# Performance work log

Measured on AMD Instinct MI355X. Metric: run time of the kernel, lower is better.

## Reference

```python
import jax, jax.numpy as jnp
import numpy as np


def setup_inputs() -> dict:
    key = jax.random.key(0)
    k1, k2, k3, k4, k5 = jax.random.split(key, 5)
    B, N, T, O, G = 32, 256, 1024, 1024, 8
    x = jax.random.normal(k1, (B, N, T), dtype=jnp.float32)
    y = jax.random.uniform(k2, (B, G), dtype=jnp.float32)  # genre mixture weights
    weight = jax.random.normal(k3, (G, O, T), dtype=jnp.float32) * (1.0 / np.sqrt(T))
    mask = jax.random.uniform(k4, (O, T), dtype=jnp.float32)
    bias = jax.random.normal(k5, (O,), dtype=jnp.float32)
    return {"x": x, "y": y, "weight": weight, "mask": mask, "bias": bias}


def reference(x, y, weight, mask, bias):
    # mask the shared weight bank: [G,O,T] * [1,O,T]
    masked_w = weight * mask[None, :, :]
    # per-sample genre-mixed weights: [B,G] x [G,O,T] -> [B,O,T]
    w_bot = jnp.einsum('bg,got->bot', y, masked_w)
    # batched masked linear: [B,N,T] x [B,O,T] -> [B,N,O], plus bias
    return jnp.einsum('bnt,bot->bno', x, w_bot) + bias
```

## Files before the change

### kernel.cpp

```cpp
#include <hip/hip_runtime.h>
#include <hip/hip_bf16.h>
#include <stdint.h>


#define B_ 32
#define N_ 256
#define T_ 1024
#define O_ 1024
#define G_ 8

#define BM 128
#define BN 128
#define BK 64

typedef __attribute__((__ext_vector_type__(8))) __bf16 bf16x8;
typedef __attribute__((__ext_vector_type__(4))) float  f32x4;

__device__ __forceinline__ unsigned short f2bf(float f) {
    union { float f; uint32_t u; } v; v.f = f;
    uint32_t u = v.u;
    uint32_t r = (u + 0x7fffu + ((u >> 16) & 1u)) >> 16;
    return (unsigned short)r;
}

#define MIX_BLOCKS (O_ * T_ / 4 / 256)
#define CVT_BLOCKS (B_ * N_ * T_ / 4 / 256)

__global__ __launch_bounds__(256) void prep_kernel(
    const float* __restrict__ w,
    const float* __restrict__ mask,
    const float* __restrict__ y,
    const float* __restrict__ x,
    unsigned short* __restrict__ Wb,
    unsigned short* __restrict__ xb)
{
    if (blockIdx.x < MIX_BLOCKS) {
        __shared__ float ys[B_ * G_];
        ys[threadIdx.x] = y[threadIdx.x];
        __syncthreads();

        const int idx = blockIdx.x * 256 + threadIdx.x;
        const int o   = idx >> 8;
        const int t4  = (idx & 255) << 2;

        const float4 m4 = *(const float4*)(mask + (size_t)o * T_ + t4);
        float4 wv[G_];
#pragma unroll
        for (int g = 0; g < G_; ++g) {
            float4 t = *(const float4*)(w + ((size_t)g * O_ + o) * T_ + t4);
            t.x *= m4.x; t.y *= m4.y; t.z *= m4.z; t.w *= m4.w;
            wv[g] = t;
        }
        unsigned short* dst = Wb + (size_t)o * T_ + t4;
#pragma unroll 4
        for (int b = 0; b < B_; ++b) {
            float ax = 0.f, ay = 0.f, az = 0.f, aw = 0.f;
#pragma unroll
            for (int g = 0; g < G_; ++g) {
                const float yv = ys[b * G_ + g];
                ax += yv * wv[g].x; ay += yv * wv[g].y;
                az += yv * wv[g].z; aw += yv * wv[g].w;
            }
            ushort4 pk;
            pk.x = f2bf(ax); pk.y = f2bf(ay); pk.z = f2bf(az); pk.w = f2bf(aw);
            *(ushort4*)(dst + (size_t)b * O_ * T_) = pk;
        }
    } else {
        const int i = (blockIdx.x - MIX_BLOCKS) * 256 + threadIdx.x;
        const float4 v = ((const float4*)x)[i];
        ushort4 pk;
        pk.x = f2bf(v.x); pk.y = f2bf(v.y); pk.z = f2bf(v.z); pk.w = f2bf(v.w);
        ((ushort4*)xb)[i] = pk;
    }
}

__device__ __forceinline__ void load16_to_lds(const unsigned short* g, unsigned short* l) {
    __builtin_amdgcn_global_load_lds(
        (const __attribute__((address_space(1))) unsigned char*)g,
        (__attribute__((address_space(3))) unsigned char*)l,
        16, 0, 0);
}

__global__ __launch_bounds__(256, 2) void gemm_kernel(
    const unsigned short* __restrict__ xb,
    const unsigned short* __restrict__ Wb,
    const float* __restrict__ bias,
    float* __restrict__ out)
{
    __shared__ __align__(16) unsigned short lA[BM * BK];
    __shared__ __align__(16) unsigned short lB[BN * BK];

    const int tn = blockIdx.x;
    const int tm = blockIdx.y;
    const int b  = blockIdx.z;

    const int tid  = threadIdx.x;
    const int lane = tid & 63;
    const int wave = tid >> 6;
    const int wm   = (wave >> 1) * 64;
    const int wn   = (wave & 1) * 64;

    const unsigned short* Ab = xb + (size_t)b * N_ * T_ + (size_t)(tm * BM) * T_;
    const unsigned short* Bb = Wb + (size_t)b * O_ * T_ + (size_t)(tn * BN) * T_;

    const int srow   = tid >> 3;
    const int schunk = (tid & 7) ^ (srow & 7);
    const unsigned short* ga0 = Ab + (size_t)srow * T_ + schunk * 8;
    const unsigned short* gb0 = Bb + (size_t)srow * T_ + schunk * 8;
    unsigned short* la_dst = lA + tid * 8;
    unsigned short* lb_dst = lB + tid * 8;

    f32x4 acc[4][4] = {};

    const int fr = lane & 15;
    const int q  = lane >> 4;
    const int sw = fr & 7;

    for (int kt = 0; kt < T_; kt += BK) {
#pragma unroll
        for (int i = 0; i < 4; ++i) {
            load16_to_lds(ga0 + kt + (size_t)(i * 32) * T_, la_dst + i * 2048);
            load16_to_lds(gb0 + kt + (size_t)(i * 32) * T_, lb_dst + i * 2048);
        }
        __syncthreads();

#pragma unroll
        for (int kk = 0; kk < 2; ++kk) {
            const int cp = ((kk * 4 + q) ^ sw) * 8;
            bf16x8 afr[4], bfr[4];
#pragma unroll
            for (int i = 0; i < 4; ++i)
                afr[i] = *(const bf16x8*)(lA + (wm + i * 16 + fr) * BK + cp);
#pragma unroll
            for (int i = 0; i < 4; ++i)
                bfr[i] = *(const bf16x8*)(lB + (wn + i * 16 + fr) * BK + cp);
#pragma unroll
            for (int mi = 0; mi < 4; ++mi)
#pragma unroll
                for (int ni = 0; ni < 4; ++ni)
                    acc[mi][ni] = __builtin_amdgcn_mfma_f32_16x16x32_bf16(
                        afr[mi], bfr[ni], acc[mi][ni], 0, 0, 0);
        }
        __syncthreads();
    }

    float* outb = out + (size_t)b * N_ * O_ + (size_t)(tm * BM) * O_ + (tn * BN);
    const int cn = lane & 15;
    const int cr = (lane >> 4) * 4;
#pragma unroll
    for (int ni = 0; ni < 4; ++ni) {
        const int col = wn + ni * 16 + cn;
        const float bv = bias[tn * BN + col];
#pragma unroll
        for (int mi = 0; mi < 4; ++mi) {
#pragma unroll
            for (int r = 0; r < 4; ++r) {
                const int row = wm + mi * 16 + cr + r;
                outb[(size_t)row * O_ + col] = acc[mi][ni][r] + bv;
            }
        }
    }
}

__global__ __launch_bounds__(256) void naive_kernel(
    const float* __restrict__ x, const float* __restrict__ y,
    const float* __restrict__ w, const float* __restrict__ mask,
    const float* __restrict__ bias, float* __restrict__ out)
{
    const int oc = blockIdx.x & 3;
    const int n  = (blockIdx.x >> 2) & (N_ - 1);
    const int b  = blockIdx.x >> 10;

    __shared__ float xs[T_];
    __shared__ float ys[G_];
    const float* xrow = x + ((size_t)b * N_ + n) * T_;
    for (int i = threadIdx.x; i < T_ / 4; i += 256)
        ((float4*)xs)[i] = ((const float4*)xrow)[i];
    if (threadIdx.x < G_) ys[threadIdx.x] = y[b * G_ + threadIdx.x];
    __syncthreads();

    const int o = oc * 256 + threadIdx.x;
    float acc = 0.f;
    for (int t = 0; t < T_; t += 4) {
        const float4 m4 = *(const float4*)(mask + (size_t)o * T_ + t);
        float4 s = {0.f, 0.f, 0.f, 0.f};
#pragma unroll
        for (int g = 0; g < G_; ++g) {
            const float4 w4 = *(const float4*)(w + ((size_t)g * O_ + o) * T_ + t);
            const float yv = ys[g];
            s.x += yv * w4.x; s.y += yv * w4.y; s.z += yv * w4.z; s.w += yv * w4.w;
        }
        acc += xs[t] * m4.x * s.x + xs[t + 1] * m4.y * s.y
             + xs[t + 2] * m4.z * s.z + xs[t + 3] * m4.w * s.w;
    }
    out[((size_t)b * N_ + n) * O_ + o] = acc + bias[o];
}

extern "C" void kernel_launch(void* const* d_in, const int* in_sizes, int n_in,
                              void* d_out, int out_size, void* d_ws, size_t ws_size,
                              hipStream_t stream) {
    const float* x    = (const float*)d_in[0];
    const float* y    = (const float*)d_in[1];
    const float* w    = (const float*)d_in[2];
    const float* mask = (const float*)d_in[3];
    const float* bias = (const float*)d_in[4];
    float* out = (float*)d_out;

    const size_t wb_bytes = (size_t)B_ * O_ * T_ * sizeof(unsigned short);
    const size_t xb_bytes = (size_t)B_ * N_ * T_ * sizeof(unsigned short);

    if (ws_size >= wb_bytes + xb_bytes) {
        unsigned short* Wb = (unsigned short*)d_ws;
        unsigned short* xb = (unsigned short*)((char*)d_ws + wb_bytes);
        prep_kernel<<<MIX_BLOCKS + CVT_BLOCKS, 256, 0, stream>>>(w, mask, y, x, Wb, xb);
        dim3 grid(O_ / BN, N_ / BM, B_);
        gemm_kernel<<<grid, 256, 0, stream>>>(xb, Wb, bias, out);
    } else {
        naive_kernel<<<B_ * N_ * (O_ / 256), 256, 0, stream>>>(x, y, w, mask, bias, out);
    }
}
```

Measured before the change: 165.3 us.

## Double-buffer GEMM LDS tiles and widen prep kernel to 8-element stores

The GEMM main loop now keeps two LDS buffers per operand and issues the global-to-LDS loads for the next K tile before computing the current one, so memory latency overlaps MFMA work. The prep kernel is reorganised so each thread handles 8 consecutive elements and writes 16-byte packed bf16 stores, and the x-conversion blocks each process 4 chunks. This launches fewer blocks. Double buffering doubles LDS use to 64KB per block, which may limit occupancy at 2 blocks per CU. The async LDS loads rely on the barrier placement for correctness.

```diff
diff --git a/kernel.cpp b/kernel.cpp
--- a/kernel.cpp
+++ b/kernel.cpp
@@ -12,6 +12,7 @@
 #define BM 128
 #define BN 128
 #define BK 64
+#define BUFSZ (BM * BK)
 
 typedef __attribute__((__ext_vector_type__(8))) __bf16 bf16x8;
 typedef __attribute__((__ext_vector_type__(4))) float  f32x4;
@@ -23,8 +24,17 @@
     return (unsigned short)r;
 }
 
-#define MIX_BLOCKS (O_ * T_ / 4 / 256)
-#define CVT_BLOCKS (B_ * N_ * T_ / 4 / 256)
+__device__ __forceinline__ uint4 pack8(const float* a) {
+    uint4 r;
+    r.x = (uint32_t)f2bf(a[0]) | ((uint32_t)f2bf(a[1]) << 16);
+    r.y = (uint32_t)f2bf(a[2]) | ((uint32_t)f2bf(a[3]) << 16);
+    r.z = (uint32_t)f2bf(a[4]) | ((uint32_t)f2bf(a[5]) << 16);
+    r.w = (uint32_t)f2bf(a[6]) | ((uint32_t)f2bf(a[7]) << 16);
+    return r;
+}
+
+#define MIXB 512
+#define CVTB 1024
 
 __global__ __launch_bounds__(256) void prep_kernel(
     const float* __restrict__ w,
@@ -34,43 +44,51 @@
     unsigned short* __restrict__ Wb,
     unsigned short* __restrict__ xb)
 {
-    if (blockIdx.x < MIX_BLOCKS) {
-        __shared__ float ys[B_ * G_];
-        ys[threadIdx.x] = y[threadIdx.x];
-        __syncthreads();
-
-        const int idx = blockIdx.x * 256 + threadIdx.x;
-        const int o   = idx >> 8;
-        const int t4  = (idx & 255) << 2;
-
-        const float4 m4 = *(const float4*)(mask + (size_t)o * T_ + t4);
-        float4 wv[G_];
+    const int tid = threadIdx.x;
+    if (blockIdx.x < MIXB) {
+        const int o = blockIdx.x * 2 + (tid >> 7);
+        const int t = (tid & 127) * 8;
+
+        const float* mp = mask + (size_t)o * T_ + t;
+        const float4 m0 = *(const float4*)(mp);
+        const float4 m1 = *(const float4*)(mp + 4);
+
+        float wv[G_][8];
 #pragma unroll
         for (int g = 0; g < G_; ++g) {
-            float4 t = *(const float4*)(w + ((size_t)g * O_ + o) * T_ + t4);
-            t.x *= m4.x; t.y *= m4.y; t.z *= m4.z; t.w *= m4.w;
-            wv[g] = t;
-        }
-        unsigned short* dst = Wb + (size_t)o * T_ + t4;
-#pragma unroll 4
+            const float* wp = w + ((size_t)g * O_ + o) * T_ + t;
+            const float4 a = *(const float4*)(wp);
+            const float4 c = *(const float4*)(wp + 4);
+            wv[g][0] = a.x * m0.x; wv[g][1] = a.y * m0.y;
+            wv[g][2] = a.z * m0.z; wv[g][3] = a.w * m0.w;
+            wv[g][4] = c.x * m1.x; wv[g][5] = c.y * m1.y;
+            wv[g][6] = c.z * m1.z; wv[g][7] = c.w * m1.w;
+        }
+        unsigned short* dst = Wb + (size_t)o * T_ + t;
         for (int b = 0; b < B_; ++b) {
-            float ax = 0.f, ay = 0.f, az = 0.f, aw = 0.f;
-#pragma unroll
-            for (int g = 0; g < G_; ++g) {
-                const float yv = ys[b * G_ + g];
-                ax += yv * wv[g].x; ay += yv * wv[g].y;
-                az += yv * wv[g].z; aw += yv * wv[g].w;
-            }
-            ushort4 pk;
-            pk.x = f2bf(ax); pk.y = f2bf(ay); pk.z = f2bf(az); pk.w = f2bf(aw);
-            *(ushort4*)(dst + (size_t)b * O_ * T_) = pk;
+            const float4 y0 = *(const float4*)(y + b * G_);
+            const float4 y1 = *(const float4*)(y + b * G_ + 4);
+            const float yv[G_] = {y0.x, y0.y, y0.z, y0.w, y1.x, y1.y, y1.z, y1.w};
+            float acc[8] = {};
+#pragma unroll
+            for (int g = 0; g < G_; ++g)
+#pragma unroll
+                for (int j = 0; j < 8; ++j)
+                    acc[j] += yv[g] * wv[g][j];
+            *(uint4*)(dst + (size_t)b * O_ * T_) = pack8(acc);
         }
     } else {
-        const int i = (blockIdx.x - MIX_BLOCKS) * 256 + threadIdx.x;
-        const float4 v = ((const float4*)x)[i];
-        ushort4 pk;
-        pk.x = f2bf(v.x); pk.y = f2bf(v.y); pk.z = f2bf(v.z); pk.w = f2bf(v.w);
-        ((ushort4*)xb)[i] = pk;
+        const int i = (blockIdx.x - MIXB) * 256 + tid;
+        const float4* x4 = (const float4*)x;
+        uint4* o4 = (uint4*)xb;
+#pragma unroll
+        for (int j = 0; j < 4; ++j) {
+            const size_t f4 = (size_t)j * 524288 + (size_t)i * 2;
+            const float4 a = x4[f4];
+            const float4 b = x4[f4 + 1];
+            const float v[8] = {a.x, a.y, a.z, a.w, b.x, b.y, b.z, b.w};
+            o4[(size_t)j * 262144 + i] = pack8(v);
+        }
     }
 }
 
@@ -87,8 +105,8 @@
     const float* __restrict__ bias,
     float* __restrict__ out)
 {
-    __shared__ __align__(16) unsigned short lA[BM * BK];
-    __shared__ __align__(16) unsigned short lB[BN * BK];
+    __shared__ __align__(16) unsigned short lA[2 * BUFSZ];
+    __shared__ __align__(16) unsigned short lB[2 * BUFSZ];
 
     const int tn = blockIdx.x;
     const int tm = blockIdx.y;
@@ -107,8 +125,17 @@
     const int schunk = (tid & 7) ^ (srow & 7);
     const unsigned short* ga0 = Ab + (size_t)srow * T_ + schunk * 8;
     const unsigned short* gb0 = Bb + (size_t)srow * T_ + schunk * 8;
-    unsigned short* la_dst = lA + tid * 8;
-    unsigned short* lb_dst = lB + tid * 8;
+
+#define STAGE(buf, kt)                                                          \
+    {                                                                           \
+        unsigned short* lad = lA + (buf) * BUFSZ + tid * 8;                     \
+        unsigned short* lbd = lB + (buf) * BUFSZ + tid * 8;                     \
+        _Pragma("unroll")                                                       \
+        for (int i_ = 0; i_ < 4; ++i_) {                                        \
+            load16_to_lds(ga0 + (kt) + (size_t)(i_ * 32) * T_, lad + i_ * 2048);\
+            load16_to_lds(gb0 + (kt) + (size_t)(i_ * 32) * T_, lbd + i_ * 2048);\
+        }                                                                       \
+    }
 
     f32x4 acc[4][4] = {};
 
@@ -116,32 +143,37 @@
     const int q  = lane >> 4;
     const int sw = fr & 7;
 
-    for (int kt = 0; kt < T_; kt += BK) {
-#pragma unroll
-        for (int i = 0; i < 4; ++i) {
-            load16_to_lds(ga0 + kt + (size_t)(i * 32) * T_, la_dst + i * 2048);
-            load16_to_lds(gb0 + kt + (size_t)(i * 32) * T_, lb_dst + i * 2048);
-        }
+#define COMPUTE(buf)                                                            \
+    {                                                                           \
+        const unsigned short* la = lA + (buf) * BUFSZ;                          \
+        const unsigned short* lb = lB + (buf) * BUFSZ;                          \
+        _Pragma("unroll")                                                       \
+        for (int kk = 0; kk < 2; ++kk) {                                        \
+            const int cp = ((kk * 4 + q) ^ sw) * 8;                             \
+            bf16x8 afr[4], bfr[4];                                              \
+            _Pragma("unroll")                                                   \
+            for (int i_ = 0; i_ < 4; ++i_)                                      \
+                afr[i_] = *(const bf16x8*)(la + (wm + i_ * 16 + fr) * BK + cp); \
+            _Pragma("unroll")                                                   \
+            for (int i_ = 0; i_ < 4; ++i_)                                      \
+                bfr[i_] = *(const bf16x8*)(lb + (wn + i_ * 16 + fr) * BK + cp); \
+            _Pragma("unroll")                                                   \
+            for (int mi = 0; mi < 4; ++mi)                                      \
+                _Pragma("unroll")                                               \
+                for (int ni = 0; ni < 4; ++ni)                                  \
+                    acc[mi][ni] = __builtin_amdgcn_mfma_f32_16x16x32_bf16(      \
+                        afr[mi], bfr[ni], acc[mi][ni], 0, 0, 0);                \
+        }                                                                       \
+    }
+
+    STAGE(0, 0)
+    for (int kt = 0; kt < T_; kt += 2 * BK) {
         __syncthreads();
-
-#pragma unroll
-        for (int kk = 0; kk < 2; ++kk) {
-            const int cp = ((kk * 4 + q) ^ sw) * 8;
-            bf16x8 afr[4], bfr[4];
-#pragma unroll
-            for (int i = 0; i < 4; ++i)
-                afr[i] = *(const bf16x8*)(lA + (wm + i * 16 + fr) * BK + cp);
-#pragma unroll
-            for (int i = 0; i < 4; ++i)
-                bfr[i] = *(const bf16x8*)(lB + (wn + i * 16 + fr) * BK + cp);
-#pragma unroll
-            for (int mi = 0; mi < 4; ++mi)
-#pragma unroll
-                for (int ni = 0; ni < 4; ++ni)
-                    acc[mi][ni] = __builtin_amdgcn_mfma_f32_16x16x32_bf16(
-                        afr[mi], bfr[ni], acc[mi][ni], 0, 0, 0);
-        }
+        STAGE(1, kt + BK)
+        COMPUTE(0)
         __syncthreads();
+        if (kt + 2 * BK < T_) STAGE(0, kt + 2 * BK)
+        COMPUTE(1)
     }
 
     float* outb = out + (size_t)b * N_ * O_ + (size_t)(tm * BM) * O_ + (tn * BN);
@@ -212,7 +244,7 @@
     if (ws_size >= wb_bytes + xb_bytes) {
         unsigned short* Wb = (unsigned short*)d_ws;
         unsigned short* xb = (unsigned short*)((char*)d_ws + wb_bytes);
-        prep_kernel<<<MIX_BLOCKS + CVT_BLOCKS, 256, 0, stream>>>(w, mask, y, x, Wb, xb);
+        prep_kernel<<<MIXB + CVTB, 256, 0, stream>>>(w, mask, y, x, Wb, xb);
         dim3 grid(O_ / BN, N_ / BM, B_);
         gemm_kernel<<<grid, 256, 0, stream>>>(xb, Wb, bias, out);
     } else {
```

After: 163.4 us. About the same (-1.2%).
